# Optimization experiments

Measured on AMD Instinct MI355X. Metric: run time of the kernel, lower is better.

## Reference

```python
import jax, jax.numpy as jnp
import numpy as np

TEMP = 0.07  # temperature used as logits / 0.07 in the original


def setup_inputs() -> dict:
    key = jax.random.key(0)
    k1, k2, k3 = jax.random.split(key, 3)
    B, N, T, L, D = 8, 128, 8, 6, 256
    meta = jax.random.normal(k1, (B, N, T, L, D), dtype=jnp.float32)
    thing = jax.random.randint(k2, (B, N, T), 0, 2, dtype=jnp.int32)
    label = jax.random.randint(k3, (B, N, T), 0, 40, dtype=jnp.int32)
    return {"meta_weight_for_con": meta, "thing_gt_idx": thing, "label_tmp": label}


def _con_loss(meta, thing, label):
    # meta: [B,N,T,L,D]; thing,label: [B,N,T]
    B, N, T, L, D = meta.shape
    P = N * T
    valid = thing.reshape(B, P).astype(bool)            # [B,P] boolean gt mask
    lab = label.reshape(B, P)                           # [B,P]
    # meta_weight_b[mask] -> [K,L,D]; permute(1,0,2) -> per-layer [K,D].
    # We keep all P positions and mask instead of compacting (jit-friendly).
    w = meta.reshape(B, P, L, D).transpose(0, 2, 1, 3)  # [B,L,P,D]
    w = w / jnp.maximum(jnp.linalg.norm(w, axis=-1, keepdims=True), 1e-12)  # F.normalize
    z = jnp.einsum('blpd,blqd->blpq', w, w) / TEMP      # similarity / temp [B,L,P,P]

    same = lab[:, :, None] == lab[:, None, :]           # [B,P,P]
    vpair = valid[:, :, None] & valid[:, None, :]
    eye = jnp.eye(P, dtype=bool)
    pos_mask = same & (~eye) & vpair                    # positives: same label, not self
    neg_mask = (~same) & vpair                          # negatives: different label

    K = valid.sum(axis=1)                               # [B] ins_num_ per batch
    pos_count = pos_mask.sum(axis=-1)                   # [B,P]
    neg_count = neg_mask.sum(axis=-1)                   # [B,P]

    # --- random positive sample per (batch, layer, row), mirroring np.random.choice ---
    u = jax.random.uniform(jax.random.key(42), (B, L, P))
    r = jnp.floor(u * pos_count[:, None, :].astype(u.dtype)).astype(jnp.int32)
    r = jnp.minimum(r, jnp.maximum(pos_count - 1, 0)[:, None, :])
    ranks = jnp.cumsum(pos_mask, axis=-1) - 1           # rank of each positive in index order
    sel = pos_mask[:, None, :, :] & (ranks[:, None, :, :] == r[..., None])  # [B,L,P,P]
    zp = jnp.sum(jnp.where(sel, z, 0.0), axis=-1)       # chosen positive logit [B,L,P]
    diag = jnp.diagonal(z, axis1=-2, axis2=-1)          # self-sim fallback when no positives
    zp = jnp.where((pos_count > 0)[:, None, :], zp, diag)

    # --- last negative (original pads by repeating the last negative to K-1) ---
    iota = jnp.arange(P)
    idx_last = jnp.max(jnp.where(neg_mask, iota[None, None, :], -1), axis=-1)  # [B,P]
    idx = jnp.broadcast_to(jnp.maximum(idx_last, 0)[:, None, :, None], (B, L, P, 1))
    zl = jnp.take_along_axis(z, idx, axis=-1)[..., 0]   # [B,L,P]

    # --- stable CE with label 0: loss = lse(logits) - zp ---
    max_n = jnp.max(jnp.where(neg_mask[:, None], z, -jnp.inf), axis=-1)  # [B,L,P]
    m = jnp.maximum(zp, max_n)
    m = jnp.where(jnp.isfinite(m), m, zp)
    sum_neg = jnp.sum(jnp.where(neg_mask[:, None], jnp.exp(z - m[..., None]), 0.0), axis=-1)
    pad = jnp.maximum((K[:, None] - 1 - neg_count), 0).astype(z.dtype)   # [B,P]
    pad_term = pad[:, None, :] * jnp.where((neg_count > 0)[:, None, :], jnp.exp(zl - m), 0.0)
    loss_row = m + jnp.log(jnp.exp(zp - m) + sum_neg + pad_term) - zp    # [B,L,P]

    row_w = valid.astype(z.dtype)
    mean_per = jnp.sum(loss_row * row_w[:, None, :], axis=-1) / jnp.maximum(K, 1)[:, None].astype(z.dtype)  # [B,L]

    gate = jnp.sum((thing.sum(axis=2) > 0), axis=1) >= 2  # skip batches with <2 gt rows
    return jnp.sum(jnp.where(gate[:, None], mean_per, 0.0))


def reference(meta_weight_for_con, thing_gt_idx, label_tmp):
    return _con_loss(meta_weight_for_con, thing_gt_idx, label_tmp)
```

## Files before the change

### kernel.cpp

```cpp
#include <hip/hip_runtime.h>
#include <stdint.h>

namespace {

constexpr int Bb = 8, Ll = 6, Dd = 256, Pp = 1024;
constexpr float SCALE_Y = 14.285714285714286f * 1.4426950408889634f;
constexpr float M0y = 21.0f;
constexpr float LN2f = 0.6931471805599453f;

typedef __attribute__((ext_vector_type(4))) float floatx4;

__device__ const int PAIRS[36] = {
  0x00,0x01,0x02,0x03,0x04,0x05,0x06,0x07,
  0x11,0x12,0x13,0x14,0x15,0x16,0x17,
  0x22,0x23,0x24,0x25,0x26,0x27,
  0x33,0x34,0x35,0x36,0x37,
  0x44,0x45,0x46,0x47,
  0x55,0x56,0x57,
  0x66,0x67,
  0x77
};

__device__ __forceinline__ void async16(const void* g, void* l) {
  __builtin_amdgcn_global_load_lds(
      (const __attribute__((address_space(1))) void*)g,
      (__attribute__((address_space(3))) void*)l, 16, 0, 0);
}

__device__ __forceinline__ uint32_t rotl32(uint32_t x, int n) {
  return (x << n) | (x >> (32 - n));
}
__device__ __forceinline__ void tf_round(uint32_t& x0, uint32_t& x1, int r) {
  x0 += x1; x1 = rotl32(x1, r); x1 ^= x0;
}
__device__ void threefry2x32(uint32_t x0, uint32_t x1, uint32_t& o0, uint32_t& o1) {
  const uint32_t k0 = 0u, k1 = 42u;
  const uint32_t k2 = k0 ^ k1 ^ 0x1BD11BDAu;
  x0 += k0; x1 += k1;
  tf_round(x0,x1,13); tf_round(x0,x1,15); tf_round(x0,x1,26); tf_round(x0,x1,6);
  x0 += k1; x1 += k2 + 1u;
  tf_round(x0,x1,17); tf_round(x0,x1,29); tf_round(x0,x1,16); tf_round(x0,x1,24);
  x0 += k2; x1 += k0 + 2u;
  tf_round(x0,x1,13); tf_round(x0,x1,15); tf_round(x0,x1,26); tf_round(x0,x1,6);
  x0 += k0; x1 += k1 + 3u;
  tf_round(x0,x1,17); tf_round(x0,x1,29); tf_round(x0,x1,16); tf_round(x0,x1,24);
  x0 += k1; x1 += k2 + 4u;
  tf_round(x0,x1,13); tf_round(x0,x1,15); tf_round(x0,x1,26); tf_round(x0,x1,6);
  x0 += k2; x1 += k0 + 5u;
  o0 = x0; o1 = x1;
}
__device__ float jax_u01(uint32_t idx) {
  const uint32_t HALF = (uint32_t)(Bb * Ll * Pp / 2);
  uint32_t o0, o1, bits;
  if (idx < HALF) { threefry2x32(idx, idx + HALF, o0, o1); bits = o0; }
  else            { threefry2x32(idx - HALF, idx, o0, o1); bits = o1; }
  return __uint_as_float((bits >> 9) | 0x3f800000u) - 1.0f;
}

__device__ __forceinline__ uint32_t fp8e4m3_rne(float x) {
  uint32_t u = __float_as_uint(x);
  const uint32_t s = (u >> 24) & 0x80u;
  u &= 0x7FFFFFFFu;
  uint32_t code;
  if (u < 0x3C800000u) {
    code = (uint32_t)__float2int_rn(__uint_as_float(u) * 512.0f);
  } else {
    const uint32_t r = (u + 0x7FFFFu + ((u >> 20) & 1u)) >> 20;
    code = r - (120u << 3);
  }
  return s | code;
}
__device__ __forceinline__ float fp8e4m3_tof(uint32_t c) {
  const uint32_t e = (c >> 3) & 15u, m = c & 7u;
  float mag;
  if (e) mag = __uint_as_float(((e + 120u) << 23) | (m << 20));
  else   mag = (float)m * 0.001953125f;
  return (c & 0x80u) ? -mag : mag;
}

__device__ __forceinline__ void fp8x4_tof(uint32_t u, float f[4]) {
#if __has_builtin(__builtin_amdgcn_cvt_f32_fp8)
  f[0] = __builtin_amdgcn_cvt_f32_fp8((int)u, 0);
  f[1] = __builtin_amdgcn_cvt_f32_fp8((int)u, 1);
  f[2] = __builtin_amdgcn_cvt_f32_fp8((int)u, 2);
  f[3] = __builtin_amdgcn_cvt_f32_fp8((int)u, 3);
#else
  f[0] = fp8e4m3_tof(u & 0xFF);
  f[1] = fp8e4m3_tof((u >> 8) & 0xFF);
  f[2] = fp8e4m3_tof((u >> 16) & 0xFF);
  f[3] = fp8e4m3_tof((u >> 24) & 0xFF);
#endif
}

constexpr int NB_NORM = Bb * Pp * Ll / 4;
constexpr int NB_ROW  = Bb * Pp / 4;

__global__ void prep_k(const float* __restrict__ meta, const int* __restrict__ thing,
                       const int* __restrict__ label, uint8_t* __restrict__ wn,
                       int* __restrict__ qpos, int* __restrict__ negc,
                       int* __restrict__ qidx, int* __restrict__ Kv,
                       int* __restrict__ gatev, float* __restrict__ rowsum_g,
                       int* __restrict__ cnt2, float* __restrict__ out) {
  __shared__ int sK[256], sG[256];
  const int bid = blockIdx.x, t = threadIdx.x;

  if (bid < NB_NORM) {
    const int wid = (bid * 256 + t) >> 6;
    const int lane = t & 63;
    const float4 v = *(const float4*)(meta + (size_t)wid * Dd + lane * 4);
    float ss = v.x * v.x + v.y * v.y + v.z * v.z + v.w * v.w;
    #pragma unroll
    for (int m = 32; m; m >>= 1) ss += __shfl_xor(ss, m, 64);
    const float inv = 1.0f / fmaxf(sqrtf(ss), 1e-12f);
    const int bp = wid / Ll, l = wid - bp * Ll;
    const int b = bp >> 10, p = bp & (Pp - 1);
    uint8_t* dst = wn + ((size_t)(b * Ll + l) * Pp + p) * Dd + lane * 4;
#if __has_builtin(__builtin_amdgcn_cvt_pk_fp8_f32)
    const int lo16 = __builtin_amdgcn_cvt_pk_fp8_f32(v.x * inv, v.y * inv, 0, false);
    const uint32_t packed =
        (uint32_t)__builtin_amdgcn_cvt_pk_fp8_f32(v.z * inv, v.w * inv, lo16, true);
#else
    const uint32_t packed = fp8e4m3_rne(v.x * inv)
                          | (fp8e4m3_rne(v.y * inv) << 8)
                          | (fp8e4m3_rne(v.z * inv) << 16)
                          | (fp8e4m3_rne(v.w * inv) << 24);
#endif
    *(uint32_t*)dst = packed;
    return;
  }
  if (bid < NB_NORM + NB_ROW) {
    const int wid = (bid - NB_NORM) * 4 + (t >> 6);
    const int lane = t & 63;
    const int b = wid >> 10, p = wid & (Pp - 1);
    const int* lab = label + b * Pp;
    const int* th  = thing + b * Pp;
    const int myLab = lab[p];
    const bool myValid = (th[p] != 0);

    uint32_t posbits = 0;
    int cnt[16];
    int pc = 0, nc = 0, last = -1;
    #pragma unroll
    for (int c = 0; c < 16; ++c) {
      const int q = c * 64 + lane;
      const int lq = lab[q];
      const bool vq = (th[q] != 0);
      const bool same = (lq == myLab);
      const bool pos = myValid && vq && same && (q != p);
      const bool neg = myValid && vq && !same;
      uint64_t bp2 = __ballot(pos);
      uint64_t bn = __ballot(neg);
      if (pos) posbits |= (1u << c);
      cnt[c] = __popcll(bp2);
      pc += cnt[c];
      nc += __popcll(bn);
      if (bn) last = c * 64 + 63 - __clzll(bn);
    }
    int qsel[Ll];
    #pragma unroll
    for (int l = 0; l < Ll; ++l) qsel[l] = p;
    if (pc > 0) {
      for (int l = 0; l < Ll; ++l) {
        const float u = jax_u01((uint32_t)((b * Ll + l) * Pp + p));
        int r = (int)floorf(u * (float)pc);
        r = min(r, pc - 1);
        int base = 0;
        for (int c = 0; c < 16; ++c) {
          if (r < base + cnt[c]) {
            const bool mine = (posbits >> c) & 1u;
            uint64_t bm = __ballot(mine);
            uint64_t ltmask = (lane == 0) ? 0ull : (~0ull >> (64 - lane));
            int myrank = __popcll(bm & ltmask);
            bool hit = mine && (base + myrank == r);
            uint64_t hb = __ballot(hit);
            qsel[l] = c * 64 + (int)__builtin_ctzll(hb);
            break;
          }
          base += cnt[c];
        }
      }
    }
    if (lane == 0) {
      negc[wid] = nc;
      qidx[wid] = (last < 0) ? 0 : last;
      #pragma unroll
      for (int l = 0; l < Ll; ++l) qpos[(b * Ll + l) * Pp + p] = qsel[l];
    }
    return;
  }
  if (bid < NB_NORM + NB_ROW + Bb) {
    const int b = bid - (NB_NORM + NB_ROW);
    int k = 0;
    for (int p = t; p < Pp; p += 256) k += (thing[b * Pp + p] != 0);
    int g = 0;
    if (t < 128) {
      int any = 0;
      for (int tt = 0; tt < 8; ++tt) any |= (thing[(b * 128 + t) * 8 + tt] != 0);
      g = any;
    }
    sK[t] = k; sG[t] = g;
    __syncthreads();
    for (int s = 128; s; s >>= 1) {
      if (t < s) { sK[t] += sK[t + s]; sG[t] += sG[t + s]; }
      __syncthreads();
    }
    if (t == 0) { Kv[b] = sK[0]; gatev[b] = (sG[0] >= 2) ? 1 : 0; }
    return;
  }
  if (bid < NB_NORM + NB_ROW + Bb + 48) {
    const int zb = bid - (NB_NORM + NB_ROW + Bb);
    const int idx = zb * 256 + t;
    *(float4*)(rowsum_g + idx * 4) = (float4){0.f, 0.f, 0.f, 0.f};
    if (zb == 0 && t < 192) { cnt2[t] = 0; cnt2[t + 192] = 0; }
    return;
  }
  if (t == 0) out[0] = 0.f;
}

__global__ __launch_bounds__(256)
void gemmfinal_k(const uint8_t* __restrict__ wn,
                 const int* __restrict__ thing, const int* __restrict__ label,
                 const int* __restrict__ qpos, const int* __restrict__ qidx,
                 const int* __restrict__ negc, const int* __restrict__ Kv,
                 const int* __restrict__ gatev, float* __restrict__ rowsum_g,
                 int* __restrict__ cnt2, float* __restrict__ out) {
  __shared__ __align__(16) uint8_t As[2 * 128 * 64];
  __shared__ __align__(16) uint8_t Bs[2 * 128 * 64];
  __shared__ int labp_s[128], valp_s[128], labq_s[128], valq_s[128];
  __shared__ float rowsum_lds[128], colsum_lds[128];
  __shared__ int fin_s[2];
  __shared__ float sb[256];

  const int t = threadIdx.x;
  const int bid = blockIdx.x;
  const int xcd = bid & 7;
  const int chunk = bid >> 3;
  const int bl = xcd + 8 * (chunk % 6);
  const int b = bl / Ll;
  const int pair = PAIRS[chunk / 6];
  const int pt = pair >> 4, qt = pair & 15;
  const bool diag = (pt == qt);
  const int p0 = pt * 128, q0 = qt * 128;

  if (t < 128) {
    labp_s[t] = label[b * Pp + p0 + t];
    valp_s[t] = thing[b * Pp + p0 + t];
    labq_s[t] = label[b * Pp + q0 + t];
    valq_s[t] = thing[b * Pp + q0 + t];
    rowsum_lds[t] = 0.f;
    colsum_lds[t] = 0.f;
  }

  const uint8_t* Wbl = wn + (size_t)bl * Pp * Dd;
  const int lane = t & 63;
  const int w = t >> 6, wr = w >> 1, wc = w & 1;
  const int cq = lane & 15, rq = lane >> 4;
  const int wbase16 = (t & ~63) * 16;

  floatx4 acc[4][4];
  #pragma unroll
  for (int i = 0; i < 4; ++i)
    #pragma unroll
    for (int j = 0; j < 4; ++j) acc[i][j] = (floatx4){0.f, 0.f, 0.f, 0.f};

  auto STAGE = [&](int bsel, int kt) {
    const int k0 = kt * 64;
    #pragma unroll
    for (int rd = 0; rd < 2; ++rd) {
      const int c = rd * 256 + t;
      const int row = c >> 2, sp2 = c & 3;
      const int sl = sp2 ^ ((row >> 1) & 3);
      async16(Wbl + (size_t)(p0 + row) * Dd + k0 + sl * 16,
              As + bsel * 8192 + rd * 4096 + wbase16);
      if (!diag)
        async16(Wbl + (size_t)(q0 + row) * Dd + k0 + sl * 16,
                Bs + bsel * 8192 + rd * 4096 + wbase16);
    }
  };

  STAGE(0, 0);
  __syncthreads();

  const uint8_t* Bbase0 = diag ? As : Bs;
  for (int kt = 0; kt < 4; ++kt) {
    const int bsel = kt & 1;
    if (kt < 3) STAGE(bsel ^ 1, kt + 1);
    const uint8_t* Ab = As + bsel * 8192;
    const uint8_t* Bb2 = Bbase0 + bsel * 8192;
    #pragma unroll
    for (int sub = 0; sub < 2; ++sub) {
      const int Lw = sub * 2 + (rq >> 1);
      const int off8 = (rq & 1) * 8;
      long long af[4], bfr[4];
      #pragma unroll
      for (int fi = 0; fi < 4; ++fi) {
        const int row = wr * 64 + fi * 16 + cq;
        af[fi] = *(const long long*)(Ab + row * 64 + (Lw ^ ((row >> 1) & 3)) * 16 + off8);
      }
      #pragma unroll
      for (int fj = 0; fj < 4; ++fj) {
        const int row = wc * 64 + fj * 16 + cq;
        bfr[fj] = *(const long long*)(Bb2 + row * 64 + (Lw ^ ((row >> 1) & 3)) * 16 + off8);
      }
      #pragma unroll
      for (int fi = 0; fi < 4; ++fi)
        #pragma unroll
        for (int fj = 0; fj < 4; ++fj)
          acc[fi][fj] = __builtin_amdgcn_mfma_f32_16x16x32_fp8_fp8(af[fi], bfr[fj],
                                                                   acc[fi][fj], 0, 0, 0);
    }
    __syncthreads();
  }

  int qlabv[4];
  float qvalf[4];
  float csum[4] = {0.f, 0.f, 0.f, 0.f};
  #pragma unroll
  for (int fj = 0; fj < 4; ++fj) {
    const int cl = wc * 64 + fj * 16 + cq;
    qlabv[fj] = labq_s[cl];
    qvalf[fj] = valq_s[cl] ? 1.f : 0.f;
  }
  #pragma unroll
  for (int fi = 0; fi < 4; ++fi) {
    #pragma unroll
    for (int reg = 0; reg < 4; ++reg) {
      const int rl = wr * 64 + fi * 16 + rq * 4 + reg;
      const int rlab = labp_s[rl];
      const float rvalf = valp_s[rl] ? 1.f : 0.f;
      float rsum = 0.f;
      #pragma unroll
      for (int fj = 0; fj < 4; ++fj) {
        const float y = acc[fi][fj][reg] * SCALE_Y;
        const float negm = (qlabv[fj] != rlab) ? (qvalf[fj] * rvalf) : 0.f;
        const float term = negm * exp2f(y - M0y);
        rsum += term;
        csum[fj] += term;
      }
      rsum += __shfl_xor(rsum, 1); rsum += __shfl_xor(rsum, 2);
      rsum += __shfl_xor(rsum, 4); rsum += __shfl_xor(rsum, 8);
      if (cq == 0) atomicAdd(&rowsum_lds[rl], rsum);
    }
  }
  if (!diag) {
    #pragma unroll
    for (int fj = 0; fj < 4; ++fj) {
      float c = csum[fj];
      c += __shfl_xor(c, 16); c += __shfl_xor(c, 32);
      if (rq == 0) atomicAdd(&colsum_lds[wc * 64 + fj * 16 + cq], c);
    }
  }
  __syncthreads();
  if (t < 128) {
    atomicAdd(&rowsum_g[bl * Pp + p0 + t], rowsum_lds[t]);
    if (!diag) atomicAdd(&rowsum_g[bl * Pp + q0 + t], colsum_lds[t]);
  }
  __syncthreads();

  if (t == 0) {
    const int n1 = __hip_atomic_fetch_add(&cnt2[bl * 8 + pt], 1,
                                          __ATOMIC_RELAXED, __HIP_MEMORY_SCOPE_AGENT);
    fin_s[0] = (n1 == 7);
    int f1 = 0;
    if (!diag) {
      const int n2 = __hip_atomic_fetch_add(&cnt2[bl * 8 + qt], 1,
                                            __ATOMIC_RELAXED, __HIP_MEMORY_SCOPE_AGENT);
      f1 = (n2 == 7);
    }
    fin_s[1] = f1;
  }
  __syncthreads();

  float accl = 0.f;
  if ((fin_s[0] | fin_s[1]) && gatev[b]) {
    const int Kb = Kv[b];
    const float invK = 1.f / (float)max(Kb, 1);
    #pragma unroll
    for (int fr = 0; fr < 2; ++fr) {
      if (!fin_s[fr]) continue;
      const int pr = fr ? qt : pt;
      const int rbase = pr * 128 + w * 32;
      for (int i = 0; i < 32; ++i) {
        const int p = rbase + i;
        if (thing[b * Pp + p] == 0) continue;
        const int qp = qpos[bl * Pp + p];
        const int qi = qidx[b * Pp + p];
        const uint32_t a4 = *(const uint32_t*)(Wbl + (size_t)p  * Dd + lane * 4);
        const uint32_t b4 = *(const uint32_t*)(Wbl + (size_t)qp * Dd + lane * 4);
        const uint32_t c4 = *(const uint32_t*)(Wbl + (size_t)qi * Dd + lane * 4);
        float fa[4], fb[4], fc[4];
        fp8x4_tof(a4, fa);
        fp8x4_tof(b4, fb);
        fp8x4_tof(c4, fc);
        float sp = 0.f, sl = 0.f;
        #pragma unroll
        for (int j = 0; j < 4; ++j) {
          sp += fa[j] * fb[j];
          sl += fa[j] * fc[j];
        }
        #pragma unroll
        for (int m = 32; m; m >>= 1) {
          sp += __shfl_xor(sp, m, 64);
          sl += __shfl_xor(sl, m, 64);
        }
        if (lane == 0) {
          const float yp = sp * SCALE_Y, yl = sl * SCALE_Y;
          const float rs = __hip_atomic_load(&rowsum_g[bl * Pp + p],
                                             __ATOMIC_RELAXED, __HIP_MEMORY_SCOPE_AGENT);
          const int nc = negc[b * Pp + p];
          const float pad = fmaxf((float)(Kb - 1 - nc), 0.f);
          const float tot = exp2f(yp - M0y) + rs + ((nc > 0) ? pad * exp2f(yl - M0y) : 0.f);
          accl += LN2f * (M0y + log2f(tot) - yp) * invK;
        }
      }
    }
  }
  sb[t] = accl;
  __syncthreads();
  for (int s = 128; s; s >>= 1) {
    if (t < s) sb[t] += sb[t + s];
    __syncthreads();
  }
  if (t == 0 && sb[0] != 0.f) atomicAdd(out, sb[0]);
}

}

extern "C" void kernel_launch(void* const* d_in, const int* in_sizes, int n_in,
                              void* d_out, int out_size, void* d_ws, size_t ws_size,
                              hipStream_t stream) {
  const float* meta = (const float*)d_in[0];
  const int* thing  = (const int*)d_in[1];
  const int* label  = (const int*)d_in[2];
  float* out = (float*)d_out;

  char* ws = (char*)d_ws;
  size_t off = 0;
  uint8_t* wn = (uint8_t*)(ws + off); off += (size_t)Bb * Ll * Pp * Dd;
  int* qpos  = (int*)(ws + off); off += (size_t)Bb * Ll * Pp * 4;
  int* negc  = (int*)(ws + off); off += (size_t)Bb * Pp * 4;
  int* qidx  = (int*)(ws + off); off += (size_t)Bb * Pp * 4;
  int* Kv    = (int*)(ws + off); off += 64;
  int* gatev = (int*)(ws + off); off += 64;
  float* rowsum_g = (float*)(ws + off); off += (size_t)Bb * Ll * Pp * 4;
  int* cnt2  = (int*)(ws + off); off += 384 * 4;

  const int nb_prep = NB_NORM + NB_ROW + Bb + 48 + 1;
  prep_k<<<nb_prep, 256, 0, stream>>>(meta, thing, label, wn, qpos, negc, qidx,
                                      Kv, gatev, rowsum_g, cnt2, out);
  gemmfinal_k<<<8 * 6 * 36, 256, 0, stream>>>(wn, thing, label, qpos, qidx, negc,
                                              Kv, gatev, rowsum_g, cnt2, out);
}
```

Baseline: 174.6 us.

## Capture positive and last-index logits from GEMM tiles instead of recomputing dot products

During the GEMM epilogue, each tile writes the scaled logit for a row's chosen positive column and its last-index column into new global buffers. The final loss pass then reads these values instead of reloading three FP8 rows and doing wave-wide dot-product reductions per valid row. This removes serialized per-row work in the finishing blocks, but adds compare branches and global atomic exchanges in the epilogue and two extra workspace arrays. zp_g and zl_g are not initialized in prep, so this relies on every valid row's target column being covered by some tile.

```diff
diff --git a/kernel.cpp b/kernel.cpp
--- a/kernel.cpp
+++ b/kernel.cpp
@@ -69,27 +69,6 @@
     code = r - (120u << 3);
   }
   return s | code;
-}
-__device__ __forceinline__ float fp8e4m3_tof(uint32_t c) {
-  const uint32_t e = (c >> 3) & 15u, m = c & 7u;
-  float mag;
-  if (e) mag = __uint_as_float(((e + 120u) << 23) | (m << 20));
-  else   mag = (float)m * 0.001953125f;
-  return (c & 0x80u) ? -mag : mag;
-}
-
-__device__ __forceinline__ void fp8x4_tof(uint32_t u, float f[4]) {
-#if __has_builtin(__builtin_amdgcn_cvt_f32_fp8)
-  f[0] = __builtin_amdgcn_cvt_f32_fp8((int)u, 0);
-  f[1] = __builtin_amdgcn_cvt_f32_fp8((int)u, 1);
-  f[2] = __builtin_amdgcn_cvt_f32_fp8((int)u, 2);
-  f[3] = __builtin_amdgcn_cvt_f32_fp8((int)u, 3);
-#else
-  f[0] = fp8e4m3_tof(u & 0xFF);
-  f[1] = fp8e4m3_tof((u >> 8) & 0xFF);
-  f[2] = fp8e4m3_tof((u >> 16) & 0xFF);
-  f[3] = fp8e4m3_tof((u >> 24) & 0xFF);
-#endif
 }
 
 constexpr int NB_NORM = Bb * Pp * Ll / 4;
@@ -223,10 +202,12 @@
                  const int* __restrict__ qpos, const int* __restrict__ qidx,
                  const int* __restrict__ negc, const int* __restrict__ Kv,
                  const int* __restrict__ gatev, float* __restrict__ rowsum_g,
+                 float* __restrict__ zp_g, float* __restrict__ zl_g,
                  int* __restrict__ cnt2, float* __restrict__ out) {
   __shared__ __align__(16) uint8_t As[2 * 128 * 64];
   __shared__ __align__(16) uint8_t Bs[2 * 128 * 64];
   __shared__ int labp_s[128], valp_s[128], labq_s[128], valq_s[128];
+  __shared__ int qpos_ps[128], qpos_qs[128], qidx_ps[128], qidx_qs[128];
   __shared__ float rowsum_lds[128], colsum_lds[128];
   __shared__ int fin_s[2];
   __shared__ float sb[256];
@@ -241,12 +222,17 @@
   const int pt = pair >> 4, qt = pair & 15;
   const bool diag = (pt == qt);
   const int p0 = pt * 128, q0 = qt * 128;
+  const int blP = bl * Pp;
 
   if (t < 128) {
     labp_s[t] = label[b * Pp + p0 + t];
     valp_s[t] = thing[b * Pp + p0 + t];
     labq_s[t] = label[b * Pp + q0 + t];
     valq_s[t] = thing[b * Pp + q0 + t];
+    qpos_ps[t] = qpos[blP + p0 + t];
+    qpos_qs[t] = qpos[blP + q0 + t];
+    qidx_ps[t] = qidx[b * Pp + p0 + t];
+    qidx_qs[t] = qidx[b * Pp + q0 + t];
     rowsum_lds[t] = 0.f;
     colsum_lds[t] = 0.f;
   }
@@ -312,22 +298,28 @@
     __syncthreads();
   }
 
-  int qlabv[4];
+  int qlabv[4], gcol[4], qq_s[4], qx_s[4], clv[4];
   float qvalf[4];
   float csum[4] = {0.f, 0.f, 0.f, 0.f};
   #pragma unroll
   for (int fj = 0; fj < 4; ++fj) {
     const int cl = wc * 64 + fj * 16 + cq;
+    clv[fj] = cl;
     qlabv[fj] = labq_s[cl];
     qvalf[fj] = valq_s[cl] ? 1.f : 0.f;
+    gcol[fj] = q0 + cl;
+    qq_s[fj] = qpos_qs[cl];
+    qx_s[fj] = qidx_qs[cl];
   }
   #pragma unroll
   for (int fi = 0; fi < 4; ++fi) {
     #pragma unroll
     for (int reg = 0; reg < 4; ++reg) {
       const int rl = wr * 64 + fi * 16 + rq * 4 + reg;
+      const int grow = p0 + rl;
       const int rlab = labp_s[rl];
       const float rvalf = valp_s[rl] ? 1.f : 0.f;
+      const int qp_r = qpos_ps[rl], qi_r = qidx_ps[rl];
       float rsum = 0.f;
       #pragma unroll
       for (int fj = 0; fj < 4; ++fj) {
@@ -336,6 +328,12 @@
         const float term = negm * exp2f(y - M0y);
         rsum += term;
         csum[fj] += term;
+        if (gcol[fj] == qp_r) atomicExch(&zp_g[blP + grow], y);
+        if (gcol[fj] == qi_r) atomicExch(&zl_g[blP + grow], y);
+        if (!diag) {
+          if (grow == qq_s[fj]) atomicExch(&zp_g[blP + gcol[fj]], y);
+          if (grow == qx_s[fj]) atomicExch(&zl_g[blP + gcol[fj]], y);
+        }
       }
       rsum += __shfl_xor(rsum, 1); rsum += __shfl_xor(rsum, 2);
       rsum += __shfl_xor(rsum, 4); rsum += __shfl_xor(rsum, 8);
@@ -347,13 +345,13 @@
     for (int fj = 0; fj < 4; ++fj) {
       float c = csum[fj];
       c += __shfl_xor(c, 16); c += __shfl_xor(c, 32);
-      if (rq == 0) atomicAdd(&colsum_lds[wc * 64 + fj * 16 + cq], c);
+      if (rq == 0) atomicAdd(&colsum_lds[wc * 64 + fj * 16 + clv[fj] - clv[fj] + cq], c);
     }
   }
   __syncthreads();
   if (t < 128) {
-    atomicAdd(&rowsum_g[bl * Pp + p0 + t], rowsum_lds[t]);
-    if (!diag) atomicAdd(&rowsum_g[bl * Pp + q0 + t], colsum_lds[t]);
+    atomicAdd(&rowsum_g[blP + p0 + t], rowsum_lds[t]);
+    if (!diag) atomicAdd(&rowsum_g[blP + q0 + t], colsum_lds[t]);
   }
   __syncthreads();
 
@@ -372,46 +370,24 @@
   __syncthreads();
 
   float accl = 0.f;
-  if ((fin_s[0] | fin_s[1]) && gatev[b]) {
+  if ((fin_s[0] | fin_s[1]) && gatev[b] && t < 128) {
     const int Kb = Kv[b];
     const float invK = 1.f / (float)max(Kb, 1);
     #pragma unroll
     for (int fr = 0; fr < 2; ++fr) {
       if (!fin_s[fr]) continue;
-      const int pr = fr ? qt : pt;
-      const int rbase = pr * 128 + w * 32;
-      for (int i = 0; i < 32; ++i) {
-        const int p = rbase + i;
-        if (thing[b * Pp + p] == 0) continue;
-        const int qp = qpos[bl * Pp + p];
-        const int qi = qidx[b * Pp + p];
-        const uint32_t a4 = *(const uint32_t*)(Wbl + (size_t)p  * Dd + lane * 4);
-        const uint32_t b4 = *(const uint32_t*)(Wbl + (size_t)qp * Dd + lane * 4);
-        const uint32_t c4 = *(const uint32_t*)(Wbl + (size_t)qi * Dd + lane * 4);
-        float fa[4], fb[4], fc[4];
-        fp8x4_tof(a4, fa);
-        fp8x4_tof(b4, fb);
-        fp8x4_tof(c4, fc);
-        float sp = 0.f, sl = 0.f;
-        #pragma unroll
-        for (int j = 0; j < 4; ++j) {
-          sp += fa[j] * fb[j];
-          sl += fa[j] * fc[j];
-        }
-        #pragma unroll
-        for (int m = 32; m; m >>= 1) {
-          sp += __shfl_xor(sp, m, 64);
-          sl += __shfl_xor(sl, m, 64);
-        }
-        if (lane == 0) {
-          const float yp = sp * SCALE_Y, yl = sl * SCALE_Y;
-          const float rs = __hip_atomic_load(&rowsum_g[bl * Pp + p],
-                                             __ATOMIC_RELAXED, __HIP_MEMORY_SCOPE_AGENT);
-          const int nc = negc[b * Pp + p];
-          const float pad = fmaxf((float)(Kb - 1 - nc), 0.f);
-          const float tot = exp2f(yp - M0y) + rs + ((nc > 0) ? pad * exp2f(yl - M0y) : 0.f);
-          accl += LN2f * (M0y + log2f(tot) - yp) * invK;
-        }
+      const int p = (fr ? qt : pt) * 128 + t;
+      if (thing[b * Pp + p] != 0) {
+        const float yp = __hip_atomic_load(&zp_g[blP + p],
+                                           __ATOMIC_RELAXED, __HIP_MEMORY_SCOPE_AGENT);
+        const float yl = __hip_atomic_load(&zl_g[blP + p],
+                                           __ATOMIC_RELAXED, __HIP_MEMORY_SCOPE_AGENT);
+        const float rs = __hip_atomic_load(&rowsum_g[blP + p],
+                                           __ATOMIC_RELAXED, __HIP_MEMORY_SCOPE_AGENT);
+        const int nc = negc[b * Pp + p];
+        const float pad = fmaxf((float)(Kb - 1 - nc), 0.f);
+        const float tot = exp2f(yp - M0y) + rs + ((nc > 0) ? pad * exp2f(yl - M0y) : 0.f);
+        accl += LN2f * (M0y + log2f(tot) - yp) * invK;
       }
     }
   }
@@ -443,11 +419,14 @@
   int* Kv    = (int*)(ws + off); off += 64;
   int* gatev = (int*)(ws + off); off += 64;
   float* rowsum_g = (float*)(ws + off); off += (size_t)Bb * Ll * Pp * 4;
+  float* zp_g     = (float*)(ws + off); off += (size_t)Bb * Ll * Pp * 4;
+  float* zl_g     = (float*)(ws + off); off += (size_t)Bb * Ll * Pp * 4;
   int* cnt2  = (int*)(ws + off); off += 384 * 4;
 
   const int nb_prep = NB_NORM + NB_ROW + Bb + 48 + 1;
   prep_k<<<nb_prep, 256, 0, stream>>>(meta, thing, label, wn, qpos, negc, qidx,
                                       Kv, gatev, rowsum_g, cnt2, out);
   gemmfinal_k<<<8 * 6 * 36, 256, 0, stream>>>(wn, thing, label, qpos, qidx, negc,
-                                              Kv, gatev, rowsum_g, cnt2, out);
-}
+                                              Kv, gatev, rowsum_g, zp_g, zl_g,
+                                              cnt2, out);
+}
```

Result: slower. 210.6 us (+20.6%).
